# Kernel tuning notes

Measured on AMD Instinct MI355X. Metric: run time of the kernel, lower is better.

The kernel has to match this reference:

```python
import jax, jax.numpy as jnp
import numpy as np

B, L, H, D = 8, 4096, 32, 128
HID = H * D          # 4096
INTER = 11008
EPS = 1e-6
ROPE_BASE = 10000.0


def setup_inputs() -> dict:
    key = jax.random.key(0)
    ks = jax.random.split(key, 11)
    s = 0.02  # weight init scale
    return {
        "hidden_states": jax.random.normal(ks[0], (B, HID), jnp.float32),
        "k_cache": jax.random.normal(ks[1], (B, L, H, D), jnp.float32),
        "v_cache": jax.random.normal(ks[2], (B, L, H, D), jnp.float32),
        "w_pack": jax.random.normal(ks[3], (3 * HID, HID), jnp.float32) * s,
        "o_proj_w": jax.random.normal(ks[4], (HID, HID), jnp.float32) * s,
        "gate_w": jax.random.normal(ks[5], (INTER, HID), jnp.float32) * s,
        "up_w": jax.random.normal(ks[6], (INTER, HID), jnp.float32) * s,
        "down_w": jax.random.normal(ks[7], (HID, INTER), jnp.float32) * s,
        "ln1_w": jnp.ones((HID,), jnp.float32),
        "ln2_w": jnp.ones((HID,), jnp.float32),
        "positions": jax.random.randint(ks[8], (B,), 0, L, jnp.int32),
    }


def _rmsnorm(x, w, eps=EPS):
    var = jnp.mean(x.astype(jnp.float32) ** 2, axis=-1, keepdims=True)
    return w * (x * jax.lax.rsqrt(var + eps))


def _rope(x, pos):
    # x: [B, H, D], pos: [B]  (GPT-NeoX style half rotation, rotary_dim == D)
    half = x.shape[-1] // 2
    inv_freq = 1.0 / (ROPE_BASE ** (jnp.arange(half, dtype=jnp.float32) / half))
    ang = pos.astype(jnp.float32)[:, None] * inv_freq[None, :]      # [B, half]
    cos = jnp.cos(ang)[:, None, :]
    sin = jnp.sin(ang)[:, None, :]
    x1, x2 = x[..., :half], x[..., half:]
    return jnp.concatenate([x1 * cos - x2 * sin, x1 * sin + x2 * cos], axis=-1)


def reference(hidden_states, k_cache, v_cache, w_pack, o_proj_w, gate_w,
              up_w, down_w, ln1_w, ln2_w, positions):
    scale = D ** -0.5
    # --- attention block ---
    h = _rmsnorm(hidden_states, ln1_w)                 # [B, HID]
    qkv = h @ w_pack.T                                 # [B, 3*HID]
    q, k, v = jnp.split(qkv, 3, axis=-1)
    q = _rope(q.reshape(B, H, D), positions)
    k = _rope(k.reshape(B, H, D), positions)
    v = v.reshape(B, H, D)
    keys = jnp.concatenate([k_cache, k[:, None]], axis=1)   # [B, L+1, H, D]
    vals = jnp.concatenate([v_cache, v[:, None]], axis=1)
    scores = jnp.einsum('bhd,blhd->bhl', q, keys) * scale   # [B, H, L+1]
    probs = jax.nn.softmax(scores, axis=-1)
    ctx = jnp.einsum('bhl,blhd->bhd', probs, vals).reshape(B, HID)
    attn_out = ctx @ o_proj_w.T
    h1 = hidden_states + attn_out
    # --- MLP block (SwiGLU) ---
    h2 = _rmsnorm(h1, ln2_w)
    mlp = (jax.nn.silu(h2 @ gate_w.T) * (h2 @ up_w.T)) @ down_w.T
    return h1 + mlp
```

## Files before the change

kernel.cpp:

```cpp
#include <hip/hip_runtime.h>
#include <math.h>

#define B_ 8
#define L_ 4096
#define H_ 32
#define D_ 128
#define HID_ 4096
#define INTER_ 11008
#define EPS_ 1e-6f

__device__ __forceinline__ float dot4(float4 a, float4 b) {
  return a.x * b.x + a.y * b.y + a.z * b.z + a.w * b.w;
}

__device__ __forceinline__ float wave_sum(float v) {
#pragma unroll
  for (int m = 32; m >= 1; m >>= 1) v += __shfl_xor(v, m, 64);
  return v;
}

__global__ __launch_bounds__(1024) void rmsnorm_kernel(const float* __restrict__ x,
                                                       const float* __restrict__ w,
                                                       float* __restrict__ out) {
  int b = blockIdx.x;
  const float4* xb = (const float4*)(x + (size_t)b * HID_);
  const float4* wp = (const float4*)w;
  float4* ob = (float4*)(out + (size_t)b * HID_);
  int tid = threadIdx.x;
  float4 v = xb[tid];
  float ss = v.x * v.x + v.y * v.y + v.z * v.z + v.w * v.w;
  ss = wave_sum(ss);
  __shared__ float red[16];
  int wid = tid >> 6, lane = tid & 63;
  if (lane == 0) red[wid] = ss;
  __syncthreads();
  float tot = 0.f;
#pragma unroll
  for (int i = 0; i < 16; i++) tot += red[i];
  float rs = rsqrtf(tot * (1.0f / (float)HID_) + EPS_);
  float4 wv = wp[tid];
  float4 o;
  o.x = v.x * rs * wv.x;
  o.y = v.y * rs * wv.y;
  o.z = v.z * rs * wv.z;
  o.w = v.w * rs * wv.w;
  ob[tid] = o;
}

template <int KD>
__global__ __launch_bounds__(256) void gemv_kernel(const float* __restrict__ W,
                                                   const float* __restrict__ x,
                                                   const float* __restrict__ res,
                                                   float* __restrict__ out,
                                                   int ostride) {
  constexpr int NF4 = KD / 4;
  int wave = ((int)blockIdx.x * 256 + (int)threadIdx.x) >> 6;
  int lane = threadIdx.x & 63;
  int n0 = wave * 2;
  const float4* w0 = (const float4*)(W + (size_t)n0 * KD);
  const float4* w1 = w0 + NF4;
  const float4* xp = (const float4*)x;
  float acc0[8] = {0.f, 0.f, 0.f, 0.f, 0.f, 0.f, 0.f, 0.f};
  float acc1[8] = {0.f, 0.f, 0.f, 0.f, 0.f, 0.f, 0.f, 0.f};
#pragma unroll 2
  for (int k4 = lane; k4 < NF4; k4 += 64) {
    float4 a0 = w0[k4];
    float4 a1 = w1[k4];
#pragma unroll
    for (int b = 0; b < 8; b++) {
      float4 xv = xp[b * NF4 + k4];
      acc0[b] += dot4(a0, xv);
      acc1[b] += dot4(a1, xv);
    }
  }
#pragma unroll
  for (int b = 0; b < 8; b++) {
    float v0 = wave_sum(acc0[b]);
    float v1 = wave_sum(acc1[b]);
    if (lane == 0) {
      size_t o = (size_t)b * ostride + n0;
      float r0 = res ? res[o] : 0.f;
      float r1 = res ? res[o + 1] : 0.f;
      out[o] = v0 + r0;
      out[o + 1] = v1 + r1;
    }
  }
}

__global__ __launch_bounds__(256) void gateup_kernel(const float* __restrict__ gW,
                                                     const float* __restrict__ uW,
                                                     const float* __restrict__ x,
                                                     float* __restrict__ act) {
  constexpr int NF4 = HID_ / 4;
  int wave = ((int)blockIdx.x * 256 + (int)threadIdx.x) >> 6;
  int lane = threadIdx.x & 63;
  int n0 = wave * 2;
  const float4* g0 = (const float4*)(gW + (size_t)n0 * HID_);
  const float4* g1 = g0 + NF4;
  const float4* u0 = (const float4*)(uW + (size_t)n0 * HID_);
  const float4* u1 = u0 + NF4;
  const float4* xp = (const float4*)x;
  float ag0[8] = {0.f, 0.f, 0.f, 0.f, 0.f, 0.f, 0.f, 0.f};
  float ag1[8] = {0.f, 0.f, 0.f, 0.f, 0.f, 0.f, 0.f, 0.f};
  float au0[8] = {0.f, 0.f, 0.f, 0.f, 0.f, 0.f, 0.f, 0.f};
  float au1[8] = {0.f, 0.f, 0.f, 0.f, 0.f, 0.f, 0.f, 0.f};
#pragma unroll 2
  for (int k4 = lane; k4 < NF4; k4 += 64) {
    float4 a0 = g0[k4], a1 = g1[k4], b0 = u0[k4], b1 = u1[k4];
#pragma unroll
    for (int b = 0; b < 8; b++) {
      float4 xv = xp[b * NF4 + k4];
      ag0[b] += dot4(a0, xv);
      ag1[b] += dot4(a1, xv);
      au0[b] += dot4(b0, xv);
      au1[b] += dot4(b1, xv);
    }
  }
#pragma unroll
  for (int b = 0; b < 8; b++) {
    float g0v = wave_sum(ag0[b]);
    float g1v = wave_sum(ag1[b]);
    float u0v = wave_sum(au0[b]);
    float u1v = wave_sum(au1[b]);
    if (lane == 0) {
      size_t o = (size_t)b * INTER_ + n0;
      act[o] = g0v / (1.f + __expf(-g0v)) * u0v;
      act[o + 1] = g1v / (1.f + __expf(-g1v)) * u1v;
    }
  }
}

__global__ __launch_bounds__(1024) void attn_kernel(const float* __restrict__ qkv,
                                                    const float* __restrict__ kc,
                                                    const float* __restrict__ vc,
                                                    const int* __restrict__ pos,
                                                    float* __restrict__ ctx) {
  int b = blockIdx.x >> 5;
  int h = blockIdx.x & 31;
  int tid = threadIdx.x;
  int wid = tid >> 6, lane = tid & 63;
  int grp = lane >> 3, j = lane & 7;

  __shared__ float s_scores[L_ + 1];
  __shared__ __align__(16) float s_q[D_];
  __shared__ __align__(16) float s_k[D_];
  __shared__ __align__(16) float s_v[D_];
  __shared__ float4 s_part[16][32];
  __shared__ float s_red[16];

  const float* qraw = qkv + (size_t)b * (3 * HID_) + h * D_;
  const float* kraw = qraw + HID_;
  const float* vraw = qraw + 2 * HID_;

  if (tid < 64) {
    float p = (float)pos[b];
    float invf = expf(-((float)tid * (1.0f / 64.0f)) * 9.210340371976184f);
    float ang = p * invf;
    float c = cosf(ang), s = sinf(ang);
    float q1 = qraw[tid], q2 = qraw[tid + 64];
    s_q[tid] = q1 * c - q2 * s;
    s_q[tid + 64] = q1 * s + q2 * c;
    float k1 = kraw[tid], k2 = kraw[tid + 64];
    s_k[tid] = k1 * c - k2 * s;
    s_k[tid + 64] = k1 * s + k2 * c;
  } else if (tid < 192) {
    int d = tid - 64;
    s_v[d] = vraw[d];
  }
  __syncthreads();

  float4 qf[4];
#pragma unroll
  for (int c = 0; c < 4; c++) qf[c] = ((const float4*)s_q)[c * 8 + j];

  const float scale = 0.08838834764831845f;

  if (tid < 8) {
    float acc = 0.f;
#pragma unroll
    for (int c = 0; c < 4; c++) acc += dot4(((const float4*)s_k)[c * 8 + tid], qf[c]);
    acc += __shfl_xor(acc, 1, 64);
    acc += __shfl_xor(acc, 2, 64);
    acc += __shfl_xor(acc, 4, 64);
    if (tid == 0) s_scores[L_] = acc * scale;
  }

  const float* kbase = kc + ((size_t)b * L_ * H_ + h) * D_;
  int l_start = wid * (L_ / 16);
#pragma unroll 2
  for (int l0 = 0; l0 < L_ / 16; l0 += 8) {
    int l = l_start + l0 + grp;
    const float4* kp = (const float4*)(kbase + (size_t)l * (H_ * D_));
    float acc = 0.f;
#pragma unroll
    for (int c = 0; c < 4; c++) acc += dot4(kp[c * 8 + j], qf[c]);
    acc += __shfl_xor(acc, 1, 64);
    acc += __shfl_xor(acc, 2, 64);
    acc += __shfl_xor(acc, 4, 64);
    if (j == 0) s_scores[l] = acc * scale;
  }
  __syncthreads();

  float mx = -1e30f;
  for (int i = tid; i < L_ + 1; i += 1024) mx = fmaxf(mx, s_scores[i]);
#pragma unroll
  for (int m = 32; m >= 1; m >>= 1) mx = fmaxf(mx, __shfl_xor(mx, m, 64));
  if (lane == 0) s_red[wid] = mx;
  __syncthreads();
#pragma unroll
  for (int i = 0; i < 16; i++) mx = fmaxf(mx, s_red[i]);
  __syncthreads();
  float lsum = 0.f;
  for (int i = tid; i < L_ + 1; i += 1024) {
    float e = __expf(s_scores[i] - mx);
    s_scores[i] = e;
    lsum += e;
  }
  lsum = wave_sum(lsum);
  if (lane == 0) s_red[wid] = lsum;
  __syncthreads();
  float sum = 0.f;
#pragma unroll
  for (int i = 0; i < 16; i++) sum += s_red[i];

  const float* vbase = vc + ((size_t)b * L_ * H_ + h) * D_;
  float4 cacc[4];
#pragma unroll
  for (int c = 0; c < 4; c++) cacc[c] = make_float4(0.f, 0.f, 0.f, 0.f);
#pragma unroll 2
  for (int l0 = 0; l0 < L_ / 16; l0 += 8) {
    int l = l_start + l0 + grp;
    float p = s_scores[l];
    const float4* vp = (const float4*)(vbase + (size_t)l * (H_ * D_));
#pragma unroll
    for (int c = 0; c < 4; c++) {
      float4 vf = vp[c * 8 + j];
      cacc[c].x += p * vf.x;
      cacc[c].y += p * vf.y;
      cacc[c].z += p * vf.z;
      cacc[c].w += p * vf.w;
    }
  }
#pragma unroll
  for (int c = 0; c < 4; c++) {
#pragma unroll
    for (int m = 8; m <= 32; m <<= 1) {
      cacc[c].x += __shfl_xor(cacc[c].x, m, 64);
      cacc[c].y += __shfl_xor(cacc[c].y, m, 64);
      cacc[c].z += __shfl_xor(cacc[c].z, m, 64);
      cacc[c].w += __shfl_xor(cacc[c].w, m, 64);
    }
  }
  if (lane < 8) {
#pragma unroll
    for (int c = 0; c < 4; c++) s_part[wid][c * 8 + lane] = cacc[c];
  }
  __syncthreads();
  if (tid < 32) {
    float4 t = s_part[0][tid];
#pragma unroll
    for (int w = 1; w < 16; w++) {
      float4 pw = s_part[w][tid];
      t.x += pw.x;
      t.y += pw.y;
      t.z += pw.z;
      t.w += pw.w;
    }
    float pn = s_scores[L_];
    float4 vn = ((const float4*)s_v)[tid];
    float inv = 1.f / sum;
    t.x = (t.x + pn * vn.x) * inv;
    t.y = (t.y + pn * vn.y) * inv;
    t.z = (t.z + pn * vn.z) * inv;
    t.w = (t.w + pn * vn.w) * inv;
    ((float4*)(ctx + (size_t)b * HID_ + h * D_))[tid] = t;
  }
}

extern "C" void kernel_launch(void* const* d_in, const int* in_sizes, int n_in,
                              void* d_out, int out_size, void* d_ws, size_t ws_size,
                              hipStream_t stream) {
  (void)in_sizes; (void)n_in; (void)out_size; (void)ws_size;
  const float* hidden = (const float*)d_in[0];
  const float* kc     = (const float*)d_in[1];
  const float* vc     = (const float*)d_in[2];
  const float* w_pack = (const float*)d_in[3];
  const float* o_w    = (const float*)d_in[4];
  const float* gate_w = (const float*)d_in[5];
  const float* up_w   = (const float*)d_in[6];
  const float* down_w = (const float*)d_in[7];
  const float* ln1    = (const float*)d_in[8];
  const float* ln2    = (const float*)d_in[9];
  const int*   pos    = (const int*)d_in[10];
  float* out = (float*)d_out;
  float* ws  = (float*)d_ws;

  float* xn  = ws;
  float* qkv = ws + 32768;
  float* ctx = ws + 131072;
  float* h1  = ws + 163840;
  float* h2  = ws + 196608;
  float* act = ws + 229376;

  rmsnorm_kernel<<<B_, 1024, 0, stream>>>(hidden, ln1, xn);
  gemv_kernel<HID_><<<1536, 256, 0, stream>>>(w_pack, xn, nullptr, qkv, 3 * HID_);
  attn_kernel<<<B_ * H_, 1024, 0, stream>>>(qkv, kc, vc, pos, ctx);
  gemv_kernel<HID_><<<512, 256, 0, stream>>>(o_w, ctx, hidden, h1, HID_);
  rmsnorm_kernel<<<B_, 1024, 0, stream>>>(h1, ln2, h2);
  gateup_kernel<<<1376, 256, 0, stream>>>(gate_w, up_w, h2, act);
  gemv_kernel<INTER_><<<512, 256, 0, stream>>>(down_w, act, h1, out, HID_);
}
```

Before: 431.6 us.

## Fuse RMSNorm into GEMVs and split attention into flash-decoding partials

Removes the standalone RMSNorm kernels by computing the sum of squares inside the QKV and gate/up GEMVs and scaling the outputs by the rsqrt factor. Attention becomes a split-K flash-decoding scheme: 8 partitions per (batch, head) run an online softmax over K and V in a single pass, and a small combine kernel merges the partials with the new token. GEMVs now compute 4 output rows per wave and use nontemporal loads for weights and KV. The aim is higher occupancy and fewer memory passes over the KV cache, at the cost of redundant norm work in every block and an extra launch.

```diff
diff --git a/kernel.cpp b/kernel.cpp
--- a/kernel.cpp
+++ b/kernel.cpp
@@ -8,153 +8,316 @@
 #define HID_ 4096
 #define INTER_ 11008
 #define EPS_ 1e-6f
-
-__device__ __forceinline__ float dot4(float4 a, float4 b) {
-  return a.x * b.x + a.y * b.y + a.z * b.z + a.w * b.w;
-}
-
+#define NP_ 8
+#define PSTRIDE_ 136
+
+typedef float f4v __attribute__((ext_vector_type(4)));
+
+__device__ __forceinline__ float dot4v(f4v a, f4v b) {
+  f4v t = a * b;
+  return t.x + t.y + t.z + t.w;
+}
 __device__ __forceinline__ float wave_sum(float v) {
 #pragma unroll
   for (int m = 32; m >= 1; m >>= 1) v += __shfl_xor(v, m, 64);
   return v;
 }
-
-__global__ __launch_bounds__(1024) void rmsnorm_kernel(const float* __restrict__ x,
-                                                       const float* __restrict__ w,
-                                                       float* __restrict__ out) {
-  int b = blockIdx.x;
-  const float4* xb = (const float4*)(x + (size_t)b * HID_);
-  const float4* wp = (const float4*)w;
-  float4* ob = (float4*)(out + (size_t)b * HID_);
-  int tid = threadIdx.x;
-  float4 v = xb[tid];
-  float ss = v.x * v.x + v.y * v.y + v.z * v.z + v.w * v.w;
-  ss = wave_sum(ss);
-  __shared__ float red[16];
-  int wid = tid >> 6, lane = tid & 63;
-  if (lane == 0) red[wid] = ss;
-  __syncthreads();
-  float tot = 0.f;
-#pragma unroll
-  for (int i = 0; i < 16; i++) tot += red[i];
-  float rs = rsqrtf(tot * (1.0f / (float)HID_) + EPS_);
-  float4 wv = wp[tid];
-  float4 o;
-  o.x = v.x * rs * wv.x;
-  o.y = v.y * rs * wv.y;
-  o.z = v.z * rs * wv.z;
-  o.w = v.w * rs * wv.w;
-  ob[tid] = o;
+__device__ __forceinline__ f4v shfl_xor4(f4v v, int mask) {
+  f4v r;
+  r.x = __shfl_xor(v.x, mask, 64);
+  r.y = __shfl_xor(v.y, mask, 64);
+  r.z = __shfl_xor(v.z, mask, 64);
+  r.w = __shfl_xor(v.w, mask, 64);
+  return r;
+}
+
+__global__ __launch_bounds__(256) void qkv_norm_gemv(const float* __restrict__ W,
+                                                     const float* __restrict__ x,
+                                                     const float* __restrict__ ln,
+                                                     float* __restrict__ out) {
+  int wave = ((int)blockIdx.x * 256 + (int)threadIdx.x) >> 6;
+  int lane = threadIdx.x & 63;
+  int n0 = wave * 4;
+  const f4v* w0 = (const f4v*)(W + (size_t)n0 * HID_);
+  const f4v* w1 = w0 + 1024;
+  const f4v* w2 = w1 + 1024;
+  const f4v* w3 = w2 + 1024;
+  const f4v* xp = (const f4v*)x;
+  const f4v* lp = (const f4v*)ln;
+  float acc0[8] = {}, acc1[8] = {}, acc2[8] = {}, acc3[8] = {}, ss[8] = {};
+#pragma unroll 2
+  for (int k4 = lane; k4 < 1024; k4 += 64) {
+    f4v a0 = __builtin_nontemporal_load(w0 + k4);
+    f4v a1 = __builtin_nontemporal_load(w1 + k4);
+    f4v a2 = __builtin_nontemporal_load(w2 + k4);
+    f4v a3 = __builtin_nontemporal_load(w3 + k4);
+    f4v lv = lp[k4];
+#pragma unroll
+    for (int b = 0; b < 8; b++) {
+      f4v xv = xp[b * 1024 + k4];
+      ss[b] += dot4v(xv, xv);
+      f4v yv = xv * lv;
+      acc0[b] += dot4v(a0, yv);
+      acc1[b] += dot4v(a1, yv);
+      acc2[b] += dot4v(a2, yv);
+      acc3[b] += dot4v(a3, yv);
+    }
+  }
+#pragma unroll
+  for (int b = 0; b < 8; b++) {
+    float s = wave_sum(ss[b]);
+    float rs = rsqrtf(s * (1.0f / (float)HID_) + EPS_);
+    float v0 = wave_sum(acc0[b]);
+    float v1 = wave_sum(acc1[b]);
+    float v2 = wave_sum(acc2[b]);
+    float v3 = wave_sum(acc3[b]);
+    if (lane == 0) {
+      float* o = out + (size_t)b * (3 * HID_) + n0;
+      o[0] = v0 * rs;
+      o[1] = v1 * rs;
+      o[2] = v2 * rs;
+      o[3] = v3 * rs;
+    }
+  }
 }
 
 template <int KD>
-__global__ __launch_bounds__(256) void gemv_kernel(const float* __restrict__ W,
-                                                   const float* __restrict__ x,
-                                                   const float* __restrict__ res,
-                                                   float* __restrict__ out,
-                                                   int ostride) {
+__global__ __launch_bounds__(256) void gemv4(const float* __restrict__ W,
+                                             const float* __restrict__ x,
+                                             const float* __restrict__ res,
+                                             float* __restrict__ out, int ostride) {
   constexpr int NF4 = KD / 4;
   int wave = ((int)blockIdx.x * 256 + (int)threadIdx.x) >> 6;
   int lane = threadIdx.x & 63;
-  int n0 = wave * 2;
-  const float4* w0 = (const float4*)(W + (size_t)n0 * KD);
-  const float4* w1 = w0 + NF4;
-  const float4* xp = (const float4*)x;
-  float acc0[8] = {0.f, 0.f, 0.f, 0.f, 0.f, 0.f, 0.f, 0.f};
-  float acc1[8] = {0.f, 0.f, 0.f, 0.f, 0.f, 0.f, 0.f, 0.f};
+  int n0 = wave * 4;
+  const f4v* w0 = (const f4v*)(W + (size_t)n0 * KD);
+  const f4v* w1 = w0 + NF4;
+  const f4v* w2 = w1 + NF4;
+  const f4v* w3 = w2 + NF4;
+  const f4v* xp = (const f4v*)x;
+  float acc0[8] = {}, acc1[8] = {}, acc2[8] = {}, acc3[8] = {};
 #pragma unroll 2
   for (int k4 = lane; k4 < NF4; k4 += 64) {
-    float4 a0 = w0[k4];
-    float4 a1 = w1[k4];
+    f4v a0 = __builtin_nontemporal_load(w0 + k4);
+    f4v a1 = __builtin_nontemporal_load(w1 + k4);
+    f4v a2 = __builtin_nontemporal_load(w2 + k4);
+    f4v a3 = __builtin_nontemporal_load(w3 + k4);
 #pragma unroll
     for (int b = 0; b < 8; b++) {
-      float4 xv = xp[b * NF4 + k4];
-      acc0[b] += dot4(a0, xv);
-      acc1[b] += dot4(a1, xv);
+      f4v xv = xp[b * NF4 + k4];
+      acc0[b] += dot4v(a0, xv);
+      acc1[b] += dot4v(a1, xv);
+      acc2[b] += dot4v(a2, xv);
+      acc3[b] += dot4v(a3, xv);
     }
   }
 #pragma unroll
   for (int b = 0; b < 8; b++) {
     float v0 = wave_sum(acc0[b]);
     float v1 = wave_sum(acc1[b]);
+    float v2 = wave_sum(acc2[b]);
+    float v3 = wave_sum(acc3[b]);
     if (lane == 0) {
       size_t o = (size_t)b * ostride + n0;
-      float r0 = res ? res[o] : 0.f;
-      float r1 = res ? res[o + 1] : 0.f;
-      out[o] = v0 + r0;
-      out[o + 1] = v1 + r1;
-    }
-  }
-}
-
-__global__ __launch_bounds__(256) void gateup_kernel(const float* __restrict__ gW,
-                                                     const float* __restrict__ uW,
-                                                     const float* __restrict__ x,
-                                                     float* __restrict__ act) {
-  constexpr int NF4 = HID_ / 4;
+      if (res) {
+        out[o + 0] = v0 + res[o + 0];
+        out[o + 1] = v1 + res[o + 1];
+        out[o + 2] = v2 + res[o + 2];
+        out[o + 3] = v3 + res[o + 3];
+      } else {
+        out[o + 0] = v0;
+        out[o + 1] = v1;
+        out[o + 2] = v2;
+        out[o + 3] = v3;
+      }
+    }
+  }
+}
+
+__global__ __launch_bounds__(256) void gateup_norm(const float* __restrict__ gW,
+                                                   const float* __restrict__ uW,
+                                                   const float* __restrict__ x,
+                                                   const float* __restrict__ ln,
+                                                   float* __restrict__ act) {
   int wave = ((int)blockIdx.x * 256 + (int)threadIdx.x) >> 6;
   int lane = threadIdx.x & 63;
   int n0 = wave * 2;
-  const float4* g0 = (const float4*)(gW + (size_t)n0 * HID_);
-  const float4* g1 = g0 + NF4;
-  const float4* u0 = (const float4*)(uW + (size_t)n0 * HID_);
-  const float4* u1 = u0 + NF4;
-  const float4* xp = (const float4*)x;
-  float ag0[8] = {0.f, 0.f, 0.f, 0.f, 0.f, 0.f, 0.f, 0.f};
-  float ag1[8] = {0.f, 0.f, 0.f, 0.f, 0.f, 0.f, 0.f, 0.f};
-  float au0[8] = {0.f, 0.f, 0.f, 0.f, 0.f, 0.f, 0.f, 0.f};
-  float au1[8] = {0.f, 0.f, 0.f, 0.f, 0.f, 0.f, 0.f, 0.f};
+  const f4v* g0 = (const f4v*)(gW + (size_t)n0 * HID_);
+  const f4v* g1 = g0 + 1024;
+  const f4v* u0 = (const f4v*)(uW + (size_t)n0 * HID_);
+  const f4v* u1 = u0 + 1024;
+  const f4v* xp = (const f4v*)x;
+  const f4v* lp = (const f4v*)ln;
+  float ag0[8] = {}, ag1[8] = {}, au0[8] = {}, au1[8] = {}, ss[8] = {};
 #pragma unroll 2
-  for (int k4 = lane; k4 < NF4; k4 += 64) {
-    float4 a0 = g0[k4], a1 = g1[k4], b0 = u0[k4], b1 = u1[k4];
+  for (int k4 = lane; k4 < 1024; k4 += 64) {
+    f4v a0 = __builtin_nontemporal_load(g0 + k4);
+    f4v a1 = __builtin_nontemporal_load(g1 + k4);
+    f4v b0 = __builtin_nontemporal_load(u0 + k4);
+    f4v b1 = __builtin_nontemporal_load(u1 + k4);
+    f4v lv = lp[k4];
 #pragma unroll
     for (int b = 0; b < 8; b++) {
-      float4 xv = xp[b * NF4 + k4];
-      ag0[b] += dot4(a0, xv);
-      ag1[b] += dot4(a1, xv);
-      au0[b] += dot4(b0, xv);
-      au1[b] += dot4(b1, xv);
+      f4v xv = xp[b * 1024 + k4];
+      ss[b] += dot4v(xv, xv);
+      f4v yv = xv * lv;
+      ag0[b] += dot4v(a0, yv);
+      ag1[b] += dot4v(a1, yv);
+      au0[b] += dot4v(b0, yv);
+      au1[b] += dot4v(b1, yv);
     }
   }
 #pragma unroll
   for (int b = 0; b < 8; b++) {
-    float g0v = wave_sum(ag0[b]);
-    float g1v = wave_sum(ag1[b]);
-    float u0v = wave_sum(au0[b]);
-    float u1v = wave_sum(au1[b]);
+    float s = wave_sum(ss[b]);
+    float rs = rsqrtf(s * (1.0f / (float)HID_) + EPS_);
+    float gv0 = wave_sum(ag0[b]) * rs;
+    float gv1 = wave_sum(ag1[b]) * rs;
+    float uv0 = wave_sum(au0[b]) * rs;
+    float uv1 = wave_sum(au1[b]) * rs;
     if (lane == 0) {
       size_t o = (size_t)b * INTER_ + n0;
-      act[o] = g0v / (1.f + __expf(-g0v)) * u0v;
-      act[o + 1] = g1v / (1.f + __expf(-g1v)) * u1v;
-    }
-  }
-}
-
-__global__ __launch_bounds__(1024) void attn_kernel(const float* __restrict__ qkv,
-                                                    const float* __restrict__ kc,
-                                                    const float* __restrict__ vc,
-                                                    const int* __restrict__ pos,
-                                                    float* __restrict__ ctx) {
-  int b = blockIdx.x >> 5;
-  int h = blockIdx.x & 31;
+      act[o + 0] = gv0 / (1.f + __expf(-gv0)) * uv0;
+      act[o + 1] = gv1 / (1.f + __expf(-gv1)) * uv1;
+    }
+  }
+}
+
+__global__ __launch_bounds__(256) void attn_part_kernel(const float* __restrict__ qkv,
+                                                        const float* __restrict__ kc,
+                                                        const float* __restrict__ vc,
+                                                        const int* __restrict__ pos,
+                                                        float* __restrict__ partials) {
+  int blk = blockIdx.x;
+  int part = blk & (NP_ - 1);
+  int bh = blk >> 3;
+  int b = bh >> 5, h = bh & 31;
   int tid = threadIdx.x;
   int wid = tid >> 6, lane = tid & 63;
   int grp = lane >> 3, j = lane & 7;
 
-  __shared__ float s_scores[L_ + 1];
   __shared__ __align__(16) float s_q[D_];
-  __shared__ __align__(16) float s_k[D_];
-  __shared__ __align__(16) float s_v[D_];
-  __shared__ float4 s_part[16][32];
-  __shared__ float s_red[16];
+  __shared__ float s_m[4], s_l[4];
+  __shared__ __align__(16) f4v s_acc[4][32];
+
+  const float* qraw = qkv + (size_t)b * (3 * HID_) + h * D_;
+  if (tid < 64) {
+    float p = (float)pos[b];
+    float invf = __expf(-((float)tid * (1.0f / 64.0f)) * 9.210340371976184f);
+    float ang = p * invf;
+    float c = cosf(ang), s = sinf(ang);
+    float q1 = qraw[tid], q2 = qraw[tid + 64];
+    s_q[tid] = q1 * c - q2 * s;
+    s_q[tid + 64] = q1 * s + q2 * c;
+  }
+  __syncthreads();
+
+  f4v qf[4];
+#pragma unroll
+  for (int c = 0; c < 4; c++) qf[c] = ((const f4v*)s_q)[c * 8 + j];
+
+  const float scale = 0.08838834764831845f;
+  const size_t rstride = H_ * D_ / 4;
+  const f4v* kb = (const f4v*)kc + ((size_t)b * L_ * H_ + h) * (D_ / 4);
+  const f4v* vb = (const f4v*)vc + ((size_t)b * L_ * H_ + h) * (D_ / 4);
+  int base = part * (L_ / NP_) + wid * (L_ / NP_ / 4);
+
+  float m = -1e30f, lsum = 0.f;
+  f4v acc[4] = {};
+#pragma unroll 2
+  for (int it = 0; it < 16; it++) {
+    int l = base + it * 8 + grp;
+    const f4v* kp = kb + (size_t)l * rstride;
+    const f4v* vp = vb + (size_t)l * rstride;
+    f4v k0 = __builtin_nontemporal_load(kp + j);
+    f4v k1 = __builtin_nontemporal_load(kp + 8 + j);
+    f4v k2 = __builtin_nontemporal_load(kp + 16 + j);
+    f4v k3 = __builtin_nontemporal_load(kp + 24 + j);
+    f4v v0 = __builtin_nontemporal_load(vp + j);
+    f4v v1 = __builtin_nontemporal_load(vp + 8 + j);
+    f4v v2 = __builtin_nontemporal_load(vp + 16 + j);
+    f4v v3 = __builtin_nontemporal_load(vp + 24 + j);
+    float s = dot4v(k0, qf[0]) + dot4v(k1, qf[1]) + dot4v(k2, qf[2]) + dot4v(k3, qf[3]);
+    s += __shfl_xor(s, 1, 64);
+    s += __shfl_xor(s, 2, 64);
+    s += __shfl_xor(s, 4, 64);
+    s *= scale;
+    if (s > m) {
+      float f = __expf(m - s);
+      lsum *= f;
+      acc[0] *= f;
+      acc[1] *= f;
+      acc[2] *= f;
+      acc[3] *= f;
+      m = s;
+    }
+    float p = __expf(s - m);
+    lsum += p;
+    acc[0] += p * v0;
+    acc[1] += p * v1;
+    acc[2] += p * v2;
+    acc[3] += p * v3;
+  }
+
+#pragma unroll
+  for (int mask = 8; mask <= 32; mask <<= 1) {
+    float m2 = __shfl_xor(m, mask, 64);
+    float l2 = __shfl_xor(lsum, mask, 64);
+    f4v a0 = shfl_xor4(acc[0], mask);
+    f4v a1 = shfl_xor4(acc[1], mask);
+    f4v a2 = shfl_xor4(acc[2], mask);
+    f4v a3 = shfl_xor4(acc[3], mask);
+    float mn = fmaxf(m, m2);
+    float f1 = __expf(m - mn), f2 = __expf(m2 - mn);
+    lsum = lsum * f1 + l2 * f2;
+    acc[0] = acc[0] * f1 + a0 * f2;
+    acc[1] = acc[1] * f1 + a1 * f2;
+    acc[2] = acc[2] * f1 + a2 * f2;
+    acc[3] = acc[3] * f1 + a3 * f2;
+    m = mn;
+  }
+  if (lane < 8) {
+#pragma unroll
+    for (int c = 0; c < 4; c++) s_acc[wid][c * 8 + lane] = acc[c];
+  }
+  if (lane == 0) {
+    s_m[wid] = m;
+    s_l[wid] = lsum;
+  }
+  __syncthreads();
+  if (tid < 32) {
+    float gm = fmaxf(fmaxf(s_m[0], s_m[1]), fmaxf(s_m[2], s_m[3]));
+    float f0 = __expf(s_m[0] - gm);
+    float f1 = __expf(s_m[1] - gm);
+    float f2 = __expf(s_m[2] - gm);
+    float f3 = __expf(s_m[3] - gm);
+    f4v a = s_acc[0][tid] * f0 + s_acc[1][tid] * f1 + s_acc[2][tid] * f2 + s_acc[3][tid] * f3;
+    float* pout = partials + ((size_t)bh * NP_ + part) * PSTRIDE_;
+    ((f4v*)pout)[tid] = a;
+    if (tid == 0) {
+      pout[128] = gm;
+      pout[129] = s_l[0] * f0 + s_l[1] * f1 + s_l[2] * f2 + s_l[3] * f3;
+    }
+  }
+}
+
+__global__ __launch_bounds__(128) void attn_combine_kernel(const float* __restrict__ qkv,
+                                                           const int* __restrict__ pos,
+                                                           const float* __restrict__ partials,
+                                                           float* __restrict__ ctx) {
+  int bh = blockIdx.x;
+  int b = bh >> 5, h = bh & 31;
+  int tid = threadIdx.x;
+
+  __shared__ float s_q[D_], s_k[D_], s_v[D_];
+  __shared__ float s_snew;
 
   const float* qraw = qkv + (size_t)b * (3 * HID_) + h * D_;
   const float* kraw = qraw + HID_;
   const float* vraw = qraw + 2 * HID_;
-
   if (tid < 64) {
     float p = (float)pos[b];
-    float invf = expf(-((float)tid * (1.0f / 64.0f)) * 9.210340371976184f);
+    float invf = __expf(-((float)tid * (1.0f / 64.0f)) * 9.210340371976184f);
     float ang = p * invf;
     float c = cosf(ang), s = sinf(ang);
     float q1 = qraw[tid], q2 = qraw[tid + 64];
@@ -163,118 +326,34 @@
     float k1 = kraw[tid], k2 = kraw[tid + 64];
     s_k[tid] = k1 * c - k2 * s;
     s_k[tid + 64] = k1 * s + k2 * c;
-  } else if (tid < 192) {
+  } else {
     int d = tid - 64;
     s_v[d] = vraw[d];
+    s_v[d + 64] = vraw[d + 64];
   }
   __syncthreads();
-
-  float4 qf[4];
-#pragma unroll
-  for (int c = 0; c < 4; c++) qf[c] = ((const float4*)s_q)[c * 8 + j];
-
-  const float scale = 0.08838834764831845f;
-
-  if (tid < 8) {
-    float acc = 0.f;
-#pragma unroll
-    for (int c = 0; c < 4; c++) acc += dot4(((const float4*)s_k)[c * 8 + tid], qf[c]);
-    acc += __shfl_xor(acc, 1, 64);
-    acc += __shfl_xor(acc, 2, 64);
-    acc += __shfl_xor(acc, 4, 64);
-    if (tid == 0) s_scores[L_] = acc * scale;
-  }
-
-  const float* kbase = kc + ((size_t)b * L_ * H_ + h) * D_;
-  int l_start = wid * (L_ / 16);
-#pragma unroll 2
-  for (int l0 = 0; l0 < L_ / 16; l0 += 8) {
-    int l = l_start + l0 + grp;
-    const float4* kp = (const float4*)(kbase + (size_t)l * (H_ * D_));
-    float acc = 0.f;
-#pragma unroll
-    for (int c = 0; c < 4; c++) acc += dot4(kp[c * 8 + j], qf[c]);
-    acc += __shfl_xor(acc, 1, 64);
-    acc += __shfl_xor(acc, 2, 64);
-    acc += __shfl_xor(acc, 4, 64);
-    if (j == 0) s_scores[l] = acc * scale;
+  if (tid < 64) {
+    float a = s_q[tid] * s_k[tid] + s_q[tid + 64] * s_k[tid + 64];
+    a = wave_sum(a);
+    if (tid == 0) s_snew = a * 0.08838834764831845f;
   }
   __syncthreads();
-
-  float mx = -1e30f;
-  for (int i = tid; i < L_ + 1; i += 1024) mx = fmaxf(mx, s_scores[i]);
-#pragma unroll
-  for (int m = 32; m >= 1; m >>= 1) mx = fmaxf(mx, __shfl_xor(mx, m, 64));
-  if (lane == 0) s_red[wid] = mx;
-  __syncthreads();
-#pragma unroll
-  for (int i = 0; i < 16; i++) mx = fmaxf(mx, s_red[i]);
-  __syncthreads();
-  float lsum = 0.f;
-  for (int i = tid; i < L_ + 1; i += 1024) {
-    float e = __expf(s_scores[i] - mx);
-    s_scores[i] = e;
-    lsum += e;
-  }
-  lsum = wave_sum(lsum);
-  if (lane == 0) s_red[wid] = lsum;
-  __syncthreads();
-  float sum = 0.f;
-#pragma unroll
-  for (int i = 0; i < 16; i++) sum += s_red[i];
-
-  const float* vbase = vc + ((size_t)b * L_ * H_ + h) * D_;
-  float4 cacc[4];
-#pragma unroll
-  for (int c = 0; c < 4; c++) cacc[c] = make_float4(0.f, 0.f, 0.f, 0.f);
-#pragma unroll 2
-  for (int l0 = 0; l0 < L_ / 16; l0 += 8) {
-    int l = l_start + l0 + grp;
-    float p = s_scores[l];
-    const float4* vp = (const float4*)(vbase + (size_t)l * (H_ * D_));
-#pragma unroll
-    for (int c = 0; c < 4; c++) {
-      float4 vf = vp[c * 8 + j];
-      cacc[c].x += p * vf.x;
-      cacc[c].y += p * vf.y;
-      cacc[c].z += p * vf.z;
-      cacc[c].w += p * vf.w;
-    }
-  }
-#pragma unroll
-  for (int c = 0; c < 4; c++) {
-#pragma unroll
-    for (int m = 8; m <= 32; m <<= 1) {
-      cacc[c].x += __shfl_xor(cacc[c].x, m, 64);
-      cacc[c].y += __shfl_xor(cacc[c].y, m, 64);
-      cacc[c].z += __shfl_xor(cacc[c].z, m, 64);
-      cacc[c].w += __shfl_xor(cacc[c].w, m, 64);
-    }
-  }
-  if (lane < 8) {
-#pragma unroll
-    for (int c = 0; c < 4; c++) s_part[wid][c * 8 + lane] = cacc[c];
-  }
-  __syncthreads();
-  if (tid < 32) {
-    float4 t = s_part[0][tid];
-#pragma unroll
-    for (int w = 1; w < 16; w++) {
-      float4 pw = s_part[w][tid];
-      t.x += pw.x;
-      t.y += pw.y;
-      t.z += pw.z;
-      t.w += pw.w;
-    }
-    float pn = s_scores[L_];
-    float4 vn = ((const float4*)s_v)[tid];
-    float inv = 1.f / sum;
-    t.x = (t.x + pn * vn.x) * inv;
-    t.y = (t.y + pn * vn.y) * inv;
-    t.z = (t.z + pn * vn.z) * inv;
-    t.w = (t.w + pn * vn.w) * inv;
-    ((float4*)(ctx + (size_t)b * HID_ + h * D_))[tid] = t;
-  }
+  float snew = s_snew;
+
+  const float* p0 = partials + (size_t)bh * NP_ * PSTRIDE_;
+  float gm = snew;
+#pragma unroll
+  for (int p = 0; p < NP_; p++) gm = fmaxf(gm, p0[p * PSTRIDE_ + 128]);
+  float fn = __expf(snew - gm);
+  float L = fn;
+  float num = fn * s_v[tid];
+#pragma unroll
+  for (int p = 0; p < NP_; p++) {
+    float f = __expf(p0[p * PSTRIDE_ + 128] - gm);
+    L += p0[p * PSTRIDE_ + 129] * f;
+    num += p0[p * PSTRIDE_ + tid] * f;
+  }
+  ctx[(size_t)b * HID_ + h * D_ + tid] = num / L;
 }
 
 extern "C" void kernel_launch(void* const* d_in, const int* in_sizes, int n_in,
@@ -295,18 +374,16 @@
   float* out = (float*)d_out;
   float* ws  = (float*)d_ws;
 
-  float* xn  = ws;
-  float* qkv = ws + 32768;
-  float* ctx = ws + 131072;
-  float* h1  = ws + 163840;
-  float* h2  = ws + 196608;
-  float* act = ws + 229376;
-
-  rmsnorm_kernel<<<B_, 1024, 0, stream>>>(hidden, ln1, xn);
-  gemv_kernel<HID_><<<1536, 256, 0, stream>>>(w_pack, xn, nullptr, qkv, 3 * HID_);
-  attn_kernel<<<B_ * H_, 1024, 0, stream>>>(qkv, kc, vc, pos, ctx);
-  gemv_kernel<HID_><<<512, 256, 0, stream>>>(o_w, ctx, hidden, h1, HID_);
-  rmsnorm_kernel<<<B_, 1024, 0, stream>>>(h1, ln2, h2);
-  gateup_kernel<<<1376, 256, 0, stream>>>(gate_w, up_w, h2, act);
-  gemv_kernel<INTER_><<<512, 256, 0, stream>>>(down_w, act, h1, out, HID_);
-}
+  float* qkv      = ws;
+  float* ctx      = ws + 98304;
+  float* h1       = ws + 131072;
+  float* act      = ws + 163840;
+  float* partials = ws + 251904;
+
+  qkv_norm_gemv<<<768, 256, 0, stream>>>(w_pack, hidden, ln1, qkv);
+  attn_part_kernel<<<B_ * H_ * NP_, 256, 0, stream>>>(qkv, kc, vc, pos, partials);
+  attn_combine_kernel<<<B_ * H_, 128, 0, stream>>>(qkv, pos, partials, ctx);
+  gemv4<HID_><<<256, 256, 0, stream>>>(o_w, ctx, hidden, h1, HID_);
+  gateup_norm<<<1376, 256, 0, stream>>>(gate_w, up_w, h1, ln2, act);
+  gemv4<INTER_><<<256, 256, 0, stream>>>(down_w, act, h1, out, HID_);
+}
```

Measured after the change: 547.5 us. 26.8% more time.
